# Kernel optimization log

Measured on AMD Instinct MI355X. Metric: run time of the kernel, lower is better.

The kernel has to match this reference:

```python
import jax, jax.numpy as jnp
import numpy as np
import math

B, N, H, NH, L, NC = 8, 128, 128, 4, 4, 1
DH = H // NH
EPS = 1e-5

def _gelu(x):
    return jax.nn.gelu(x, approximate=False)  # torch nn.GELU default is exact erf

def _ln(x, g, b):
    m = x.mean(-1, keepdims=True)
    v = ((x - m) ** 2).mean(-1, keepdims=True)
    return (x - m) / jnp.sqrt(v + EPS) * g + b

def _bn(x, mask, g, b):
    # BatchNorm1d over valid (unpadded) nodes only, batch statistics (train mode)
    m = mask[..., None].astype(x.dtype)
    cnt = m.sum()
    mu = (x * m).sum((0, 1)) / cnt
    var = (((x - mu) ** 2) * m).sum((0, 1)) / cnt
    return (x - mu) / jnp.sqrt(var + EPS) * g + b

def _forward(e, u, atom_emb, bond_emb, eigw_W, eigw_b, mha_norm_g, mha_norm_b, qkv_W, qkv_b, out_W, out_b, ffn_norm_g, ffn_norm_b, ffn1_W, ffn1_b, ffn2_W, ffn2_b, dec_W, dec_b, fe1_W, fe1_b, fe2_W, fe2_b, pre_W, pre_b, f1_W, f1_b, bn1_g, bn1_b, f2_W, f2_b, bn2_g, bn2_b, lin_W, lin_b, node_feat, edge_feat, length):
    Bx, Nx = e.shape
    node_mask = jnp.arange(Nx)[None, :] < length[:, None]                        # [B,N]
    edge_mask = (node_mask[:, :, None] & node_mask[:, None, :]).astype(e.dtype)  # [B,src,dst]
    # SineEncoding
    div = jnp.exp(jnp.arange(0, H, 2, dtype=e.dtype) * (-math.log(10000.0) / H))
    pe = (e * 100.0)[:, :, None] * div
    eeig = jnp.concatenate([e[..., None], jnp.sin(pe), jnp.cos(pe)], axis=-1)    # [B,N,H+1]
    eig = eeig @ eigw_W.T + eigw_b                                               # [B,N,H]
    # multi-head self-attention over eigenvalue tokens with key padding mask
    xm = _ln(eig, mha_norm_g, mha_norm_b)
    qkv = xm @ qkv_W.T + qkv_b
    q, k, v = jnp.split(qkv, 3, axis=-1)
    q = q.reshape(Bx, Nx, NH, DH).transpose(0, 2, 1, 3)
    k = k.reshape(Bx, Nx, NH, DH).transpose(0, 2, 1, 3)
    v = v.reshape(Bx, Nx, NH, DH).transpose(0, 2, 1, 3)
    scores = jnp.einsum('bhqd,bhkd->bhqk', q, k) / math.sqrt(DH)
    scores = jnp.where(node_mask[:, None, None, :], scores, -jnp.inf)
    attn = jax.nn.softmax(scores, axis=-1)                                       # [B,NH,N,N]
    ctx = jnp.einsum('bhqk,bhkd->bhqd', attn, v).transpose(0, 2, 1, 3).reshape(Bx, Nx, H)
    eig = eig + (ctx @ out_W.T + out_b)
    y = _ln(eig, ffn_norm_g, ffn_norm_b)
    y = _gelu(y @ ffn1_W.T + ffn1_b) @ ffn2_W.T + ffn2_b
    eig = eig + y
    new_e = (eig @ dec_W.T + dec_b).transpose(0, 2, 1)                           # [B,NH,N]
    # spectral bases: identity + u @ diag(new_e_k) @ u^T per head, as fused diagonal scale
    filters = jnp.einsum('bnm,bkm,bpm->bnpk', u, new_e, u)                       # [B,N,N,NH]
    eye = jnp.broadcast_to(jnp.eye(Nx, dtype=e.dtype)[None, :, :, None], (Bx, Nx, Nx, 1))
    bases = jnp.concatenate([eye, filters], axis=-1)                             # [B,N,N,NH+1]
    bases = _gelu(_gelu(bases @ fe1_W.T + fe1_b) @ fe2_W.T + fe2_b)              # [B,N,N,H]
    xf = atom_emb[node_feat]                                                     # [B,N,H]
    ea = bond_emb[edge_feat]                                                     # [B,N,N,H]
    for l in range(L):
        # copy_u gather + per-edge FFN * bases + masked scatter-sum to dst
        msg = _gelu((xf[:, :, None, :] + ea) @ pre_W[l].T + pre_b[l]) * bases
        aggr = jnp.einsum('bijh,bij->bjh', msg, edge_mask)
        xf = xf + aggr
        y = xf @ f1_W[l].T + f1_b[l]
        y = jax.nn.relu(_bn(y, node_mask, bn1_g[l], bn1_b[l]))
        y = y @ f2_W[l].T + f2_b[l]
        y = jax.nn.relu(_bn(y, node_mask, bn2_g[l], bn2_b[l]))
        xf = xf + y
    nm = node_mask[..., None].astype(e.dtype)
    h = (xf * nm).sum(1) / length[:, None].astype(e.dtype)                       # AvgPooling over valid nodes
    h = h @ lin_W.T + lin_b
    return h, new_e, attn

def setup_inputs():
    key = jax.random.key(0)
    ks = iter(jax.random.split(key, 64))
    def w(*shape):
        return jax.random.normal(next(ks), shape, dtype=jnp.float32) * 0.02
    z = lambda *s: jnp.zeros(s, dtype=jnp.float32)
    o = lambda *s: jnp.ones(s, dtype=jnp.float32)
    e = jax.random.uniform(next(ks), (B, N), dtype=jnp.float32) * 2.0
    u = jnp.linalg.qr(jax.random.normal(next(ks), (B, N, N), dtype=jnp.float32))[0]
    inp = {
        'e': e, 'u': u,
        'atom_emb': w(40, H), 'bond_emb': w(10, H).at[0].set(0.0),
        'eigw_W': w(H, H + 1), 'eigw_b': z(H),
        'mha_norm_g': o(H), 'mha_norm_b': z(H),
        'qkv_W': w(3 * H, H), 'qkv_b': z(3 * H),
        'out_W': w(H, H), 'out_b': z(H),
        'ffn_norm_g': o(H), 'ffn_norm_b': z(H),
        'ffn1_W': w(H, H), 'ffn1_b': z(H),
        'ffn2_W': w(H, H), 'ffn2_b': z(H),
        'dec_W': w(NH, H), 'dec_b': z(NH),
        'fe1_W': w(H, NH + 1), 'fe1_b': z(H),
        'fe2_W': w(H, H), 'fe2_b': z(H),
        'pre_W': w(L, H, H), 'pre_b': z(L, H),
        'f1_W': w(L, H, H), 'f1_b': z(L, H),
        'bn1_g': o(L, H), 'bn1_b': z(L, H),
        'f2_W': w(L, H, H), 'f2_b': z(L, H),
        'bn2_g': o(L, H), 'bn2_b': z(L, H),
        'lin_W': w(NC, H), 'lin_b': z(NC),
        'node_feat': jax.random.randint(next(ks), (B, N), 0, 40),
        'edge_feat': jax.random.randint(next(ks), (B, N, N), 0, 10),
        'length': 64 + jax.random.randint(next(ks), (B,), 0, N - 63),
    }
    return inp

def reference(e, u, atom_emb, bond_emb, eigw_W, eigw_b, mha_norm_g, mha_norm_b, qkv_W, qkv_b, out_W, out_b, ffn_norm_g, ffn_norm_b, ffn1_W, ffn1_b, ffn2_W, ffn2_b, dec_W, dec_b, fe1_W, fe1_b, fe2_W, fe2_b, pre_W, pre_b, f1_W, f1_b, bn1_g, bn1_b, f2_W, f2_b, bn2_g, bn2_b, lin_W, lin_b, node_feat, edge_feat, length):
    return _forward(e, u, atom_emb, bond_emb, eigw_W, eigw_b, mha_norm_g, mha_norm_b, qkv_W, qkv_b, out_W, out_b, ffn_norm_g, ffn_norm_b, ffn1_W, ffn1_b, ffn2_W, ffn2_b, dec_W, dec_b, fe1_W, fe1_b, fe2_W, fe2_b, pre_W, pre_b, f1_W, f1_b, bn1_g, bn1_b, f2_W, f2_b, bn2_g, bn2_b, lin_W, lin_b, node_feat, edge_feat, length)
```

## Files before the change

### kernel.cpp

```cpp
#include <hip/hip_runtime.h>
#include <hip/hip_bf16.h>
#include <math.h>

#define BB 8
#define NN 128
#define HH 128
#define NHD 4
#define DHD 32
#define LAY 4
#define EPSV 1e-5f

typedef __hip_bfloat16 bf16;
typedef unsigned short ushortt;
typedef short bf16x8 __attribute__((ext_vector_type(8)));
typedef float f32x4 __attribute__((ext_vector_type(4)));

__device__ __forceinline__ float b2f(bf16 x){ return __bfloat162float(x); }
__device__ __forceinline__ bf16 f2b(float x){ return __float2bfloat16(x); }
__device__ __forceinline__ ushortt f2us(float x){ bf16 b=__float2bfloat16(x); return *(ushortt*)&b; }
__device__ __forceinline__ float gelu_f(float x){ return 0.5f*x*(1.0f+erff(x*0.7071067811865476f)); }
__device__ __forceinline__ float gelu_h(float x){
  float t = 0.7978845608028654f*x*(1.0f + 0.044715f*x*x);
  float e = __expf(2.0f*t);
  float th = 1.0f - 2.0f/(e + 1.0f);
  return 0.5f*x*(1.0f + th);
}
__device__ __forceinline__ float erf_fast(float x){
  float ax = fabsf(x);
  float t = __builtin_amdgcn_rcpf(__builtin_fmaf(0.3275911f, ax, 1.0f));
  float p = __builtin_fmaf(1.061405429f, t, -1.453152027f);
  p = __builtin_fmaf(p, t, 1.421413741f);
  p = __builtin_fmaf(p, t, -0.284496736f);
  p = __builtin_fmaf(p, t, 0.254829592f);
  p = p*t;
  float e = __expf(-ax*ax);
  float y = __builtin_fmaf(-p, e, 1.0f);
  return __builtin_copysignf(y, x);
}
__device__ __forceinline__ float gelu_fe(float x){
  return 0.5f*x*(1.0f + erf_fast(x*0.7071067811865476f));
}


__global__ __launch_bounds__(256) void k_prep(const float* __restrict__ fe2W,
    const float* __restrict__ preW, const float* __restrict__ eigW,
    const float* __restrict__ qkvW, const float* __restrict__ outW,
    const float* __restrict__ ffn1W, const float* __restrict__ ffn2W,
    const float* __restrict__ f1W, const float* __restrict__ f2W,
    const float* __restrict__ aemb, const int* __restrict__ nf,
    const float* __restrict__ bemb, const float* __restrict__ preb,
    ushortt* __restrict__ wbf, float* __restrict__ gs, float* __restrict__ xf0,
    float* __restrict__ eigWT, float* __restrict__ qkvWT, float* __restrict__ outWT,
    float* __restrict__ ffn1WT, float* __restrict__ ffn2WT,
    float* __restrict__ f1WT, float* __restrict__ f2WT,
    float* __restrict__ bondWall){
  int idx = blockIdx.x*256 + threadIdx.x;
  if (idx < 10240) gs[idx] = 0.f;
  if (idx < 81920){
    float v = (idx < 16384) ? fe2W[idx] : preW[idx - 16384];
    wbf[idx] = f2us(v);
  }
  if (idx < 131072){
    int node = idx >> 7, h2 = idx & 127;
    xf0[idx] = aemb[nf[node]*HH + h2];
  }
  if (idx < 16512){ int o = idx/129, kq = idx - o*129; eigWT[kq*128+o] = eigW[idx]; }
  if (idx < 49152){ int o = idx>>7, m = idx&127; qkvWT[m*384+o] = qkvW[idx]; }
  if (idx < 16384){ int o = idx>>7, m = idx&127;
    outWT[m*128+o]  = outW[idx];
    ffn1WT[m*128+o] = ffn1W[idx];
    ffn2WT[m*128+o] = ffn2W[idx];
  }
  if (idx < 65536){ int l = idx>>14, r = idx&16383; int o = r>>7, m = r&127;
    f1WT[l*16384 + m*128+o] = f1W[idx];
    f2WT[l*16384 + m*128+o] = f2W[idx];
  }
  if (idx < 5120){
    int l = idx / 1280; int r = idx - l*1280; int e2 = r >> 7; int hcol = r & 127;
    const float* br = bemb + e2*128;
    const float* wr = preW + l*16384 + hcol*128;
    float acc = preb[l*128 + hcol];
    for (int m=0;m<128;m++) acc += br[m]*wr[m];
    bondWall[idx] = acc;
  }
}


__global__ void k_fe_a(const float* __restrict__ e, const float* __restrict__ eigWT,
                       const float* __restrict__ eigb, const float* __restrict__ g,
                       const float* __restrict__ bt, const float* __restrict__ qkvWT,
                       const float* __restrict__ qkvb,
                       float* __restrict__ eigout, float* __restrict__ q,
                       float* __restrict__ kT, float* __restrict__ v){
  int row = blockIdx.x; int tid = threadIdx.x;
  int b = row >> 7, n = row & 127;
  __shared__ float ee[129]; __shared__ float buf[128]; __shared__ float xm[128];
  float ev = e[row];
  if (tid < 64){
    float dv = expf(-0.1439115683121279f * (float)tid);
    float pe = ev * 100.0f * dv;
    ee[1+tid] = sinf(pe);
    ee[65+tid] = cosf(pe);
  }
  if (tid == 0) ee[0] = ev;
  __syncthreads();
  float x = eigb[tid];
  for (int k2=0;k2<129;k2++) x += ee[k2]*eigWT[k2*128+tid];
  eigout[row*HH+tid] = x;
  buf[tid]=x; __syncthreads();
  for (int s2=64;s2>0;s2>>=1){ if(tid<s2) buf[tid]+=buf[tid+s2]; __syncthreads(); }
  float mean = buf[0]*(1.0f/128.0f); __syncthreads();
  float d = x-mean; buf[tid]=d*d; __syncthreads();
  for (int s2=64;s2>0;s2>>=1){ if(tid<s2) buf[tid]+=buf[tid+s2]; __syncthreads(); }
  float var = buf[0]*(1.0f/128.0f);
  xm[tid] = d*rsqrtf(var+EPSV)*g[tid]+bt[tid];
  __syncthreads();
  #pragma unroll
  for (int s3=0;s3<3;s3++){
    float acc = qkvb[s3*HH+tid];
    const float* wt = qkvWT + s3*HH + tid;
    for (int m=0;m<HH;m++) acc += xm[m]*wt[m*384];
    if (s3==0) q[row*HH+tid]=acc;
    else if (s3==1) kT[b*16384 + tid*128 + n]=acc;
    else v[row*HH+tid]=acc;
  }
}

__global__ __launch_bounds__(512) void k_attc(const float* __restrict__ q,
    const float* __restrict__ kT, const float* __restrict__ v,
    const float* __restrict__ eig, const int* __restrict__ length,
    const float* __restrict__ outWT, const float* __restrict__ outb,
    const float* __restrict__ fng, const float* __restrict__ fnb,
    const float* __restrict__ w1T, const float* __restrict__ b1,
    const float* __restrict__ w2T, const float* __restrict__ b2,
    const float* __restrict__ dW, const float* __restrict__ db,
    float* __restrict__ newe, float* __restrict__ outp){
  int row = blockIdx.x; int b = row>>7, qi = row&127;
  int tid = threadIdx.x;
  int hg = tid>>7, lt = tid&127;
  int len = length[b];
  __shared__ float qv[4][DHD];
  __shared__ float red[4][128];
  __shared__ float satt[4][128];
  __shared__ float part[4][128];
  __shared__ float sc[128], sbuf[128], sxm[128], stt[128], sx[128];
  if (lt < DHD) qv[hg][lt] = q[(b*NN+qi)*HH + hg*DHD + lt];
  __syncthreads();
  float s = -1e30f;
  if (lt < len){
    const float* kr = kT + b*16384 + hg*DHD*128 + lt;
    float scr=0.f;
    for (int d2=0; d2<DHD; d2++) scr += qv[hg][d2]*kr[d2*128];
    s = scr * 0.17677669529663687f;
  }
  red[hg][lt]=s; __syncthreads();
  for (int st=64;st>0;st>>=1){ if(lt<st) red[hg][lt]=fmaxf(red[hg][lt],red[hg][lt+st]); __syncthreads(); }
  float mx = red[hg][0]; __syncthreads();
  float pp = (lt<len)? expf(s-mx):0.0f;
  red[hg][lt]=pp; __syncthreads();
  for (int st=64;st>0;st>>=1){ if(lt<st) red[hg][lt]+=red[hg][lt+st]; __syncthreads(); }
  float a = pp / red[hg][0];
  satt[hg][lt] = a;
  outp[4104 + ((b*NHD+hg)*NN+qi)*NN + lt] = a;
  __syncthreads();
  {
    int hd = lt>>5;
    float p=0.f;
    for (int j=hg*32; j<hg*32+32; j++) p += satt[hd][j]*v[(b*NN+j)*HH+lt];
    part[hg][lt]=p;
  }
  __syncthreads();
  if (tid < 128) sc[tid] = (part[0][tid]+part[1][tid])+(part[2][tid]+part[3][tid]);
  __syncthreads();
  {
    float p = (hg==0)? outb[lt] : 0.f;
    for (int m=hg*32; m<hg*32+32; m++) p += sc[m]*outWT[m*128+lt];
    part[hg][lt]=p;
  }
  __syncthreads();
  if (tid < 128){
    float x = eig[row*HH+tid] + ((part[0][tid]+part[1][tid])+(part[2][tid]+part[3][tid]));
    sx[tid] = x; sbuf[tid] = x;
  }
  __syncthreads();
  for (int s2=64;s2>0;s2>>=1){ if(tid<s2) sbuf[tid]+=sbuf[tid+s2]; __syncthreads(); }
  float mean = sbuf[0]*(1.f/128.f); __syncthreads();
  if (tid < 128){ float d = sx[tid]-mean; sbuf[tid]=d*d; }
  __syncthreads();
  for (int s2=64;s2>0;s2>>=1){ if(tid<s2) sbuf[tid]+=sbuf[tid+s2]; __syncthreads(); }
  float var = sbuf[0]*(1.f/128.f);
  if (tid < 128){
    float d = sx[tid]-mean;
    sxm[tid] = d*rsqrtf(var+EPSV)*fng[tid]+fnb[tid];
  }
  __syncthreads();
  {
    float p = (hg==0)? b1[lt] : 0.f;
    for (int m=hg*32; m<hg*32+32; m++) p += sxm[m]*w1T[m*128+lt];
    part[hg][lt]=p;
  }
  __syncthreads();
  if (tid < 128) stt[tid]=gelu_f((part[0][tid]+part[1][tid])+(part[2][tid]+part[3][tid]));
  __syncthreads();
  {
    float p = (hg==0)? b2[lt] : 0.f;
    for (int m=hg*32; m<hg*32+32; m++) p += stt[m]*w2T[m*128+lt];
    part[hg][lt]=p;
  }
  __syncthreads();
  if (tid < 128) sx[tid] = sx[tid] + ((part[0][tid]+part[1][tid])+(part[2][tid]+part[3][tid]));
  __syncthreads();
  if (tid < 4){
    float acc = db[tid];
    const float* wr = dW + tid*HH;
    for (int h2=0;h2<HH;h2++) acc += sx[h2]*wr[h2];
    int idx=(b*NHD+tid)*NN+qi;
    newe[idx]=acc; outp[8+idx]=acc;
  }
}

__global__ __launch_bounds__(256) void k_fe2(const float* __restrict__ u,
    const float* __restrict__ newe,
    const float* __restrict__ w1g, const float* __restrict__ b1g,
    const ushortt* __restrict__ w2bf, const float* __restrict__ b2g,
    const int* __restrict__ length,
    bf16* __restrict__ bases){
  int blk = blockIdx.x;
  int bi = blk >> 1;
  int r0 = (blk & 1)*64;
  int b = bi >> 7;
  int nloc = bi & 127;
  int len = length[b];
  if (nloc >= len || r0 >= len) return;
  int tid = threadIdx.x;
  int lane = tid & 63, w = tid >> 6, quad = lane >> 4, l15 = lane & 15;
  int pr = r0 + w*16 + l15;
  __shared__ alignas(16) ushortt sW2[128*128];
  __shared__ float w1a[128*4];
  __shared__ float w1b[128*2];
  __shared__ float b2s[128];
  __shared__ float cn[4][128];
  for (int idx = tid; idx < 2048; idx += 256){
    int r = idx >> 4, cb = idx & 15;
    *(uint4*)&sW2[r*128 + ((cb*8) ^ ((r&15)<<3))] = *(const uint4*)&w2bf[r*128 + cb*8];
  }
  if (tid < 128){
    w1a[tid*4+0] = b1g[tid];
    w1a[tid*4+1] = w1g[tid*5+0];
    w1a[tid*4+2] = w1g[tid*5+1];
    w1a[tid*4+3] = w1g[tid*5+2];
    w1b[tid*2+0] = w1g[tid*5+3];
    w1b[tid*2+1] = w1g[tid*5+4];
    b2s[tid] = b2g[tid];
  }
  for (int idx = tid; idx < 512; idx += 256){
    int k = idx >> 7, m = idx & 127;
    cn[k][m] = u[(b*NN+nloc)*NN + m] * newe[(b*NHD+k)*NN + m];
  }
  __syncthreads();
  bool wact = (r0 + w*16) < len;
  f32x4 acc[8];
  #pragma unroll
  for (int nt=0;nt<8;nt++) acc[nt] = (f32x4){0.f,0.f,0.f,0.f};
  if (wact){
    float f0=0.f, f1=0.f, f2v=0.f, f3=0.f;
    const float4* ur = (const float4*)(u + ((size_t)b*NN + pr)*NN);
    for (int m4 = quad*8; m4 < quad*8+8; m4++){
      float4 uv = ur[m4];
      int m = m4*4;
      f0 += cn[0][m]*uv.x; f0 += cn[0][m+1]*uv.y; f0 += cn[0][m+2]*uv.z; f0 += cn[0][m+3]*uv.w;
      f1 += cn[1][m]*uv.x; f1 += cn[1][m+1]*uv.y; f1 += cn[1][m+2]*uv.z; f1 += cn[1][m+3]*uv.w;
      f2v += cn[2][m]*uv.x; f2v += cn[2][m+1]*uv.y; f2v += cn[2][m+2]*uv.z; f2v += cn[2][m+3]*uv.w;
      f3 += cn[3][m]*uv.x; f3 += cn[3][m+1]*uv.y; f3 += cn[3][m+2]*uv.z; f3 += cn[3][m+3]*uv.w;
    }
    f0 += __shfl_xor(f0, 16, 64);  f0 += __shfl_xor(f0, 32, 64);
    f1 += __shfl_xor(f1, 16, 64);  f1 += __shfl_xor(f1, 32, 64);
    f2v += __shfl_xor(f2v, 16, 64); f2v += __shfl_xor(f2v, 32, 64);
    f3 += __shfl_xor(f3, 16, 64);  f3 += __shfl_xor(f3, 32, 64);
    float dg = (pr == nloc) ? 1.0f : 0.0f;
    for (int kk = 0; kk < 128; kk += 32){
      bf16x8 af;
      #pragma unroll
      for (int j=0;j<8;j++){
        int m = kk + quad*8 + j;
        const float4 wa = *(const float4*)&w1a[m*4];
        const float2 wb = *(const float2*)&w1b[m*2];
        float a = wa.x + wa.y*dg + wa.z*f0 + wa.w*f1 + wb.x*f2v + wb.y*f3;
        af[j] = (short)f2us(gelu_fe(a));
      }
      #pragma unroll
      for (int nt=0;nt<8;nt++){
        int rowb = nt*16 + l15;
        int off = (kk + quad*8) ^ (l15 << 3);
        bf16x8 bfr = *(const bf16x8*)&sW2[rowb*128 + off];
        acc[nt] = __builtin_amdgcn_mfma_f32_16x16x32_bf16(af, bfr, acc[nt], 0, 0, 0);
      }
    }
  }
  __syncthreads();
  ushortt* sT = sW2;
  if (wact){
    #pragma unroll
    for (int nt=0;nt<8;nt++){
      int h = nt*16 + l15;
      float bb = b2s[h];
      #pragma unroll
      for (int reg=0;reg<4;reg++){
        int lr = w*16 + quad*4 + reg;
        sT[lr*132 + h] = f2us(gelu_fe(acc[nt][reg] + bb));
      }
    }
  }
  __syncthreads();
  int rmax = len - r0; if (rmax > 64) rmax = 64;
  ushort4* gout = (ushort4*)(bases + (size_t)bi*16384 + r0*128);
  for (int idx = tid; idx < rmax*32; idx += 256){
    int row = idx >> 5, seg = idx & 31;
    gout[idx] = *(const ushort4*)&sT[row*132 + seg*4];
  }
}


__global__ __launch_bounds__(256) void k_xwl2(const float* __restrict__ xfprev,
    const float* __restrict__ t2, const float* __restrict__ gsum2p,
    const float* __restrict__ gsq2p, const float* __restrict__ g2p,
    const float* __restrict__ bb2p, const int* __restrict__ length, int prevapply,
    const ushortt* __restrict__ wbfl, float* __restrict__ xfB,
    float* __restrict__ xfW){
  int blk = blockIdx.x;
  int b = blk >> 2, rq = blk & 3;
  int tid = threadIdx.x;
  int lane = tid & 63, w = tid >> 6, quad = lane >> 4, l15 = lane & 15;
  __shared__ alignas(16) ushortt sA[32*136];
  __shared__ float smu[128], sistd[128], sg[128], sbb[128];
  if (prevapply && tid < 128){
    float cnt = 0.f;
    for (int q2=0;q2<BB;q2++) cnt += (float)length[q2];
    float mu = gsum2p[tid]/cnt;
    float var = gsq2p[tid]/cnt - mu*mu;
    smu[tid]=mu; sistd[tid]=rsqrtf(fmaxf(var,0.0f)+EPSV);
    sg[tid]=g2p[tid]; sbb[tid]=bb2p[tid];
  }
  __syncthreads();
  for (int idx = tid; idx < 1024; idx += 256){
    int r = idx >> 5, c = idx & 31;
    int gr = b*128 + rq*32 + r;
    float4 xv = ((const float4*)xfprev)[gr*32 + c];
    if (prevapply){
      float4 tv = ((const float4*)t2)[gr*32 + c];
      int f0 = c*4;
      xv.x += fmaxf((tv.x-smu[f0+0])*sistd[f0+0]*sg[f0+0]+sbb[f0+0], 0.f);
      xv.y += fmaxf((tv.y-smu[f0+1])*sistd[f0+1]*sg[f0+1]+sbb[f0+1], 0.f);
      xv.z += fmaxf((tv.z-smu[f0+2])*sistd[f0+2]*sg[f0+2]+sbb[f0+2], 0.f);
      xv.w += fmaxf((tv.w-smu[f0+3])*sistd[f0+3]*sg[f0+3]+sbb[f0+3], 0.f);
      ((float4*)xfB)[gr*32 + c] = xv;
    }
    ushort4 o;
    o.x=f2us(xv.x); o.y=f2us(xv.y); o.z=f2us(xv.z); o.w=f2us(xv.w);
    *(ushort4*)&sA[r*136 + c*4] = o;
  }
  __syncthreads();
  f32x4 acc[2][2];
  #pragma unroll
  for (int mt=0;mt<2;mt++)
    #pragma unroll
    for (int nt=0;nt<2;nt++) acc[mt][nt] = (f32x4){0.f,0.f,0.f,0.f};
  #pragma unroll
  for (int kk = 0; kk < 128; kk += 32){
    bf16x8 af[2], bfr[2];
    #pragma unroll
    for (int mt=0;mt<2;mt++) af[mt] = *(const bf16x8*)&sA[(mt*16+l15)*136 + kk + quad*8];
    #pragma unroll
    for (int nt=0;nt<2;nt++) bfr[nt] = *(const bf16x8*)&wbfl[((w*2+nt)*16+l15)*128 + kk + quad*8];
    #pragma unroll
    for (int mt=0;mt<2;mt++)
      #pragma unroll
      for (int nt=0;nt<2;nt++)
        acc[mt][nt] = __builtin_amdgcn_mfma_f32_16x16x32_bf16(af[mt], bfr[nt], acc[mt][nt], 0, 0, 0);
  }
  #pragma unroll
  for (int mt=0;mt<2;mt++)
    #pragma unroll
    for (int nt=0;nt<2;nt++){
      int h = (w*2+nt)*16 + l15;
      #pragma unroll
      for (int reg=0;reg<4;reg++){
        int prr = rq*32 + mt*16 + quad*4 + reg;
        xfW[(b*128 + prr)*128 + h] = acc[mt][nt][reg];
      }
    }
}

__global__ __launch_bounds__(512) void k_edge(const float* __restrict__ xfin, float* __restrict__ xfout,
    const bf16* __restrict__ bases, const float* __restrict__ xfW,
    const float* __restrict__ bondWl, const int* __restrict__ ef,
    const int* __restrict__ length,
    const float* __restrict__ w1t, const float* __restrict__ bias1,
    float* __restrict__ t1, float* __restrict__ gst){
  int bj = blockIdx.x; int b = bj >> 7, j = bj & 127;
  int len = length[b];
  int tid = threadIdx.x; int h = tid & 127, ih = tid >> 7;
  __shared__ float sBW[10][128];
  __shared__ int sEf[128];
  __shared__ float part[4][128];
  for (int idx = tid; idx < 1280; idx += 512) sBW[idx>>7][idx&127] = bondWl[idx];
  if (tid < 128) sEf[tid] = ef[(b*NN + tid)*NN + j];
  __syncthreads();
  float agg = 0.f;
  if (j < len){
    const float* xwb = xfW + b*NN*HH + h;
    const bf16* bb = bases + ((size_t)b*NN + j)*NN*HH + h;
    for (int i = ih; i < len; i += 4){
      float vv = gelu_h(xwb[i*128] + sBW[sEf[i]][h]);
      agg += vv * b2f(bb[i*128]);
    }
  }
  part[ih][h] = agg; __syncthreads();
  if (tid < 128){
    int o = (b*NN + j)*HH + tid;
    float xrow = xfin[o] + part[0][tid] + part[1][tid] + part[2][tid] + part[3][tid];
    xfout[o] = xrow;
    part[0][tid] = xrow;
  }
  __syncthreads();
  float acc = (ih==0) ? bias1[h] : 0.f;
  {
    const float* wcol = w1t + h;
    int m0 = ih*32;
    for (int m = m0; m < m0+32; m++) acc += part[0][m]*wcol[m*128];
  }
  float* red = &sBW[0][0];
  __syncthreads();
  red[ih*128 + h] = acc; __syncthreads();
  if (tid < 128){
    float t1v = red[tid] + red[128+tid] + red[256+tid] + red[384+tid];
    t1[(b*NN + j)*HH + tid] = t1v;
    if (j < len){
      int bank = bj & 7;
      atomicAdd(&gst[bank*256 + tid], t1v);
      atomicAdd(&gst[bank*256 + 128 + tid], t1v*t1v);
    }
  }
}

__global__ __launch_bounds__(256) void k_g2s(const float* __restrict__ t1,
    const float* __restrict__ gstL,
    const float* __restrict__ g1, const float* __restrict__ bb1,
    const float* __restrict__ w2t, const float* __restrict__ bias2,
    const int* __restrict__ length, float* __restrict__ t2){
  int blk = blockIdx.x; int tid = threadIdx.x;
  int f = tid & 127, rh = tid >> 7;
  __shared__ float sy[4][128];
  __shared__ float red1[2][128], red2[2][128];
  int r0 = blk*4;
  float cnt = 0.f;
  for (int b=0;b<BB;b++) cnt += (float)length[b];
  float su = 0.f, sq = 0.f;
  #pragma unroll
  for (int k=0;k<8;k++){ su += gstL[k*256 + f]; sq += gstL[k*256 + 128 + f]; }
  float mu = su/cnt;
  float var = sq/cnt - mu*mu;
  float istd = rsqrtf(fmaxf(var,0.0f)+EPSV);
  float gg = g1[f], bbv = bb1[f];
  for (int idx = tid; idx < 512; idx += 256){
    int r = idx >> 7;
    float x = t1[(r0+r)*128 + f];
    float y = (x-mu)*istd*gg + bbv;
    sy[r][f] = fmaxf(y, 0.0f);
  }
  __syncthreads();
  float bsv = bias2[f];
  float s=0.f, s2=0.f;
  for (int rr = rh*2; rr < rh*2+2; rr++){
    int rg = r0 + rr; int b = rg >> 7, n = rg & 127;
    float acc = bsv;
    for (int m=0;m<128;m++) acc += sy[rr][m]*w2t[m*128+f];
    t2[rg*128+f] = acc;
    if (n < length[b]){ s += acc; s2 += acc*acc; }
  }
  red1[rh][f]=s; red2[rh][f]=s2; __syncthreads();
  if (tid < 128){
    atomicAdd((float*)&gstL[2048 + tid], red1[0][tid]+red1[1][tid]);
    atomicAdd((float*)&gstL[2048 + 128 + tid], red2[0][tid]+red2[1][tid]);
  }
}

__global__ void k_pool2(const float* __restrict__ xf, const float* __restrict__ t2,
                        const float* __restrict__ gsum2, const float* __restrict__ gsq2,
                        const float* __restrict__ g2, const float* __restrict__ bb2,
                        const int* __restrict__ length,
                        const float* lw, const float* lb, float* __restrict__ outp){
  int b = blockIdx.x, tid=threadIdx.x;
  int len = length[b];
  float cnt = 0.f;
  for (int q2=0;q2<BB;q2++) cnt += (float)length[q2];
  float mu = gsum2[tid]/cnt;
  float var = gsq2[tid]/cnt - mu*mu;
  float istd = rsqrtf(fmaxf(var,0.0f)+EPSV);
  float gg = g2[tid], bbv = bb2[tid];
  float s=0.f;
  for (int n2=0;n2<len;n2++){
    int o = (b*NN+n2)*HH+tid;
    float x = xf[o] + fmaxf((t2[o]-mu)*istd*gg+bbv, 0.0f);
    s += x;
  }
  s /= (float)len;
  __shared__ float red[128];
  red[tid]=s*lw[tid]; __syncthreads();
  for (int st=64;st>0;st>>=1){ if(tid<st) red[tid]+=red[tid+st]; __syncthreads(); }
  if (tid==0) outp[b]=red[0]+lb[0];
}


extern "C" void kernel_launch(void* const* d_in, const int* in_sizes, int n_in,
                              void* d_out, int out_size, void* d_ws, size_t ws_size,
                              hipStream_t stream) {
  (void)in_sizes; (void)n_in; (void)out_size; (void)ws_size;
  const float* e        = (const float*)d_in[0];
  const float* u        = (const float*)d_in[1];
  const float* atom_emb = (const float*)d_in[2];
  const float* bond_emb = (const float*)d_in[3];
  const float* eigw_W   = (const float*)d_in[4];
  const float* eigw_b   = (const float*)d_in[5];
  const float* mng      = (const float*)d_in[6];
  const float* mnb      = (const float*)d_in[7];
  const float* qkvW     = (const float*)d_in[8];
  const float* qkvb     = (const float*)d_in[9];
  const float* outW     = (const float*)d_in[10];
  const float* outb     = (const float*)d_in[11];
  const float* fng      = (const float*)d_in[12];
  const float* fnb      = (const float*)d_in[13];
  const float* ffn1W    = (const float*)d_in[14];
  const float* ffn1b    = (const float*)d_in[15];
  const float* ffn2W    = (const float*)d_in[16];
  const float* ffn2b    = (const float*)d_in[17];
  const float* decW     = (const float*)d_in[18];
  const float* decb     = (const float*)d_in[19];
  const float* fe1W     = (const float*)d_in[20];
  const float* fe1b     = (const float*)d_in[21];
  const float* fe2W     = (const float*)d_in[22];
  const float* fe2b     = (const float*)d_in[23];
  const float* preW     = (const float*)d_in[24];
  const float* preb     = (const float*)d_in[25];
  const float* f1W      = (const float*)d_in[26];
  const float* f1b      = (const float*)d_in[27];
  const float* bn1g     = (const float*)d_in[28];
  const float* bn1b     = (const float*)d_in[29];
  const float* f2W      = (const float*)d_in[30];
  const float* f2b      = (const float*)d_in[31];
  const float* bn2g     = (const float*)d_in[32];
  const float* bn2b     = (const float*)d_in[33];
  const float* linW     = (const float*)d_in[34];
  const float* linb     = (const float*)d_in[35];
  const int* nodef      = (const int*)d_in[36];
  const int* edgef      = (const int*)d_in[37];
  const int* length     = (const int*)d_in[38];

  float* outp = (float*)d_out;

  char* p = (char*)d_ws;
  auto alloc = [&](size_t bytes)->void*{ void* r=(void*)p; p += (bytes+255)&~(size_t)255; return r; };
  const int TOK = BB*NN*HH;
  float* eig   = (float*)alloc(TOK*4);
  float* q     = (float*)alloc(TOK*4);
  float* kT    = (float*)alloc(TOK*4);
  float* v     = (float*)alloc(TOK*4);
  float* newe  = (float*)alloc(BB*NHD*NN*4);
  bf16*  bases = (bf16*) alloc((size_t)BB*NN*NN*HH*2);
  float* xf0   = (float*)alloc(TOK*4);
  float* xfB   = (float*)alloc(TOK*4);
  float* xfC   = (float*)alloc(TOK*4);
  float* xfD   = (float*)alloc(TOK*4);
  float* t1    = (float*)alloc(TOK*4);
  float* t2    = (float*)alloc(TOK*4);
  float* xfW   = (float*)alloc(TOK*4);
  float* gs    = (float*)alloc(10240*4);
  ushortt* wbf = (ushortt*)alloc(81920*2);
  float* eigWT = (float*)alloc(16512*4);
  float* qkvWT = (float*)alloc(49152*4);
  float* outWT = (float*)alloc(16384*4);
  float* ffn1WT= (float*)alloc(16384*4);
  float* ffn2WT= (float*)alloc(16384*4);
  float* f1WT  = (float*)alloc(65536*4);
  float* f2WT  = (float*)alloc(65536*4);
  float* bondWall = (float*)alloc(5120*4);

  k_prep<<<512, 256, 0, stream>>>(fe2W, preW, eigw_W, qkvW, outW, ffn1W, ffn2W,
                                  f1W, f2W, atom_emb, nodef, bond_emb, preb,
                                  wbf, gs, xf0, eigWT, qkvWT, outWT, ffn1WT,
                                  ffn2WT, f1WT, f2WT, bondWall);

  k_fe_a<<<BB*NN, 128, 0, stream>>>(e, eigWT, eigw_b, mng, mnb, qkvWT, qkvb, eig, q, kT, v);
  k_attc<<<BB*NN, 512, 0, stream>>>(q, kT, v, eig, length,
                                    outWT, outb, fng, fnb,
                                    ffn1WT, ffn1b, ffn2WT, ffn2b,
                                    decW, decb, newe, outp);

  k_fe2<<<2*BB*NN, 256, 0, stream>>>(u, newe, fe1W, fe1b, wbf, fe2b, length, bases);

  const float* xfprev = xf0;
  float* xfcur = xfC;
  for (int l=0;l<LAY;l++){
    const ushortt* wbfl = wbf + 16384 + l*16384;
    float* gsl = gs + l*2560;
    float* gsp = gs + (l-1)*2560;
    k_xwl2<<<BB*4, 256, 0, stream>>>(xfprev, t2,
                                   (l>0)? gsp+2048 : gs, (l>0)? gsp+2048+128 : gs,
                                   bn2g + (l>0? (l-1)*HH:0), bn2b + (l>0? (l-1)*HH:0),
                                   length, (l>0)?1:0,
                                   wbfl, xfB, xfW);
    const float* xin = (l==0)? xf0 : xfB;
    k_edge<<<BB*NN, 512, 0, stream>>>(xin, xfcur, bases, xfW, bondWall + l*1280,
                                      edgef, length,
                                      f1WT + l*16384, f1b + l*HH, t1, gsl);
    k_g2s<<<256, 256, 0, stream>>>(t1, gsl, bn1g + l*HH, bn1b + l*HH,
                                   f2WT + l*16384, f2b + l*HH, length, t2);
    xfprev = xfcur;
    xfcur = (xfcur == xfC) ? xfD : xfC;
  }
  k_pool2<<<BB, 128, 0, stream>>>(xfprev, t2, gs+3*2560+2048, gs+3*2560+2048+128,
                                  bn2g + 3*HH, bn2b + 3*HH, length, linW, linb, outp);
}
```

Before: 397.9 us.

## Merge prep with front encoder and fold layer-0 projection into basis kernel

The weight-prep kernel and the eigen-encoding/QKV kernel become one launch. Extra blocks handle two rows each and read the original untransposed eig and qkv weights, so the transposes of those two matrices are dropped. The layer-0 bf16 MFMA projection (xf0 × pre_W) is appended as extra blocks to the basis-construction kernel. That removes the layer-0 launch of k_xwl2 and its runtime prevapply branch. Fewer launches and less serialisation are traded for strided per-thread weight reads in the encoder part.

Measured after the change: 390.3 us. Within noise of the previous version (-1.9%).

```diff
diff --git a/kernel.cpp b/kernel.cpp
--- a/kernel.cpp
+++ b/kernel.cpp
@@ -42,87 +42,89 @@
 }
 
 
-__global__ __launch_bounds__(256) void k_prep(const float* __restrict__ fe2W,
-    const float* __restrict__ preW, const float* __restrict__ eigW,
-    const float* __restrict__ qkvW, const float* __restrict__ outW,
-    const float* __restrict__ ffn1W, const float* __restrict__ ffn2W,
-    const float* __restrict__ f1W, const float* __restrict__ f2W,
-    const float* __restrict__ aemb, const int* __restrict__ nf,
-    const float* __restrict__ bemb, const float* __restrict__ preb,
+__global__ __launch_bounds__(256) void k_front(
+    const float* __restrict__ fe2W, const float* __restrict__ preW,
+    const float* __restrict__ outW, const float* __restrict__ ffn1W,
+    const float* __restrict__ ffn2W, const float* __restrict__ f1W,
+    const float* __restrict__ f2W, const float* __restrict__ aemb,
+    const int* __restrict__ nf, const float* __restrict__ bemb,
+    const float* __restrict__ preb,
     ushortt* __restrict__ wbf, float* __restrict__ gs, float* __restrict__ xf0,
-    float* __restrict__ eigWT, float* __restrict__ qkvWT, float* __restrict__ outWT,
-    float* __restrict__ ffn1WT, float* __restrict__ ffn2WT,
-    float* __restrict__ f1WT, float* __restrict__ f2WT,
-    float* __restrict__ bondWall){
-  int idx = blockIdx.x*256 + threadIdx.x;
-  if (idx < 10240) gs[idx] = 0.f;
-  if (idx < 81920){
-    float v = (idx < 16384) ? fe2W[idx] : preW[idx - 16384];
-    wbf[idx] = f2us(v);
-  }
-  if (idx < 131072){
-    int node = idx >> 7, h2 = idx & 127;
-    xf0[idx] = aemb[nf[node]*HH + h2];
-  }
-  if (idx < 16512){ int o = idx/129, kq = idx - o*129; eigWT[kq*128+o] = eigW[idx]; }
-  if (idx < 49152){ int o = idx>>7, m = idx&127; qkvWT[m*384+o] = qkvW[idx]; }
-  if (idx < 16384){ int o = idx>>7, m = idx&127;
-    outWT[m*128+o]  = outW[idx];
-    ffn1WT[m*128+o] = ffn1W[idx];
-    ffn2WT[m*128+o] = ffn2W[idx];
-  }
-  if (idx < 65536){ int l = idx>>14, r = idx&16383; int o = r>>7, m = r&127;
-    f1WT[l*16384 + m*128+o] = f1W[idx];
-    f2WT[l*16384 + m*128+o] = f2W[idx];
-  }
-  if (idx < 5120){
-    int l = idx / 1280; int r = idx - l*1280; int e2 = r >> 7; int hcol = r & 127;
-    const float* br = bemb + e2*128;
-    const float* wr = preW + l*16384 + hcol*128;
-    float acc = preb[l*128 + hcol];
-    for (int m=0;m<128;m++) acc += br[m]*wr[m];
-    bondWall[idx] = acc;
-  }
-}
-
-
-__global__ void k_fe_a(const float* __restrict__ e, const float* __restrict__ eigWT,
-                       const float* __restrict__ eigb, const float* __restrict__ g,
-                       const float* __restrict__ bt, const float* __restrict__ qkvWT,
-                       const float* __restrict__ qkvb,
-                       float* __restrict__ eigout, float* __restrict__ q,
-                       float* __restrict__ kT, float* __restrict__ v){
-  int row = blockIdx.x; int tid = threadIdx.x;
+    float* __restrict__ outWT, float* __restrict__ ffn1WT, float* __restrict__ ffn2WT,
+    float* __restrict__ f1WT, float* __restrict__ f2WT, float* __restrict__ bondWall,
+    const float* __restrict__ e, const float* __restrict__ eigW,
+    const float* __restrict__ eigb, const float* __restrict__ g,
+    const float* __restrict__ bt, const float* __restrict__ qkvW,
+    const float* __restrict__ qkvb,
+    float* __restrict__ eigout, float* __restrict__ q,
+    float* __restrict__ kT, float* __restrict__ v){
+  int blk = blockIdx.x;
+  int tid = threadIdx.x;
+  if (blk < 512){
+    int idx = blk*256 + tid;
+    if (idx < 10240) gs[idx] = 0.f;
+    if (idx < 81920){
+      float vv = (idx < 16384) ? fe2W[idx] : preW[idx - 16384];
+      wbf[idx] = f2us(vv);
+    }
+    if (idx < 131072){
+      int node = idx >> 7, h2 = idx & 127;
+      xf0[idx] = aemb[nf[node]*HH + h2];
+    }
+    if (idx < 16384){ int o = idx>>7, m = idx&127;
+      outWT[m*128+o]  = outW[idx];
+      ffn1WT[m*128+o] = ffn1W[idx];
+      ffn2WT[m*128+o] = ffn2W[idx];
+    }
+    if (idx < 65536){ int l = idx>>14, r = idx&16383; int o = r>>7, m = r&127;
+      f1WT[l*16384 + m*128+o] = f1W[idx];
+      f2WT[l*16384 + m*128+o] = f2W[idx];
+    }
+    if (idx < 5120){
+      int l = idx / 1280; int r = idx - l*1280; int e2 = r >> 7; int hcol = r & 127;
+      const float* br = bemb + e2*128;
+      const float* wr = preW + l*16384 + hcol*128;
+      float acc = preb[l*128 + hcol];
+      for (int m=0;m<128;m++) acc += br[m]*wr[m];
+      bondWall[idx] = acc;
+    }
+    return;
+  }
+  int sub = tid >> 7, lt = tid & 127;
+  int row = (blk - 512)*2 + sub;
   int b = row >> 7, n = row & 127;
-  __shared__ float ee[129]; __shared__ float buf[128]; __shared__ float xm[128];
+  __shared__ float ee[2][129]; __shared__ float buf[2][128]; __shared__ float xm[2][128];
   float ev = e[row];
-  if (tid < 64){
-    float dv = expf(-0.1439115683121279f * (float)tid);
+  if (lt < 64){
+    float dv = expf(-0.1439115683121279f * (float)lt);
     float pe = ev * 100.0f * dv;
-    ee[1+tid] = sinf(pe);
-    ee[65+tid] = cosf(pe);
-  }
-  if (tid == 0) ee[0] = ev;
-  __syncthreads();
-  float x = eigb[tid];
-  for (int k2=0;k2<129;k2++) x += ee[k2]*eigWT[k2*128+tid];
-  eigout[row*HH+tid] = x;
-  buf[tid]=x; __syncthreads();
-  for (int s2=64;s2>0;s2>>=1){ if(tid<s2) buf[tid]+=buf[tid+s2]; __syncthreads(); }
-  float mean = buf[0]*(1.0f/128.0f); __syncthreads();
-  float d = x-mean; buf[tid]=d*d; __syncthreads();
-  for (int s2=64;s2>0;s2>>=1){ if(tid<s2) buf[tid]+=buf[tid+s2]; __syncthreads(); }
-  float var = buf[0]*(1.0f/128.0f);
-  xm[tid] = d*rsqrtf(var+EPSV)*g[tid]+bt[tid];
+    ee[sub][1+lt] = sinf(pe);
+    ee[sub][65+lt] = cosf(pe);
+  }
+  if (lt == 0) ee[sub][0] = ev;
+  __syncthreads();
+  float x = eigb[lt];
+  {
+    const float* er = eigW + lt*129;
+    for (int k2=0;k2<129;k2++) x += ee[sub][k2]*er[k2];
+  }
+  eigout[row*HH+lt] = x;
+  buf[sub][lt]=x; __syncthreads();
+  for (int s2=64;s2>0;s2>>=1){ if(lt<s2) buf[sub][lt]+=buf[sub][lt+s2]; __syncthreads(); }
+  float mean = buf[sub][0]*(1.0f/128.0f); __syncthreads();
+  float d = x-mean; buf[sub][lt]=d*d; __syncthreads();
+  for (int s2=64;s2>0;s2>>=1){ if(lt<s2) buf[sub][lt]+=buf[sub][lt+s2]; __syncthreads(); }
+  float var = buf[sub][0]*(1.0f/128.0f);
+  xm[sub][lt] = d*rsqrtf(var+EPSV)*g[lt]+bt[lt];
   __syncthreads();
   #pragma unroll
   for (int s3=0;s3<3;s3++){
-    float acc = qkvb[s3*HH+tid];
-    const float* wt = qkvWT + s3*HH + tid;
-    for (int m=0;m<HH;m++) acc += xm[m]*wt[m*384];
-    if (s3==0) q[row*HH+tid]=acc;
-    else if (s3==1) kT[b*16384 + tid*128 + n]=acc;
-    else v[row*HH+tid]=acc;
+    float acc = qkvb[s3*HH+lt];
+    const float* wt = qkvW + (s3*HH + lt)*128;
+    for (int m=0;m<HH;m++) acc += xm[sub][m]*wt[m];
+    if (s3==0) q[row*HH+lt]=acc;
+    else if (s3==1) kT[b*16384 + lt*128 + n]=acc;
+    else v[row*HH+lt]=acc;
   }
 }
 
@@ -219,27 +221,74 @@
   }
 }
 
-__global__ __launch_bounds__(256) void k_fe2(const float* __restrict__ u,
+__global__ __launch_bounds__(256) void k_bx(const float* __restrict__ u,
     const float* __restrict__ newe,
     const float* __restrict__ w1g, const float* __restrict__ b1g,
     const ushortt* __restrict__ w2bf, const float* __restrict__ b2g,
     const int* __restrict__ length,
-    bf16* __restrict__ bases){
+    bf16* __restrict__ bases,
+    const float* __restrict__ xf0, const ushortt* __restrict__ wbfl0,
+    float* __restrict__ xfW){
   int blk = blockIdx.x;
+  int tid = threadIdx.x;
+  int lane = tid & 63, w = tid >> 6, quad = lane >> 4, l15 = lane & 15;
+  __shared__ alignas(16) char us[38400];
+  if (blk >= 2048){
+    int blk2 = blk - 2048;
+    int b = blk2 >> 2, rq = blk2 & 3;
+    ushortt* sA = (ushortt*)us;
+    for (int idx = tid; idx < 1024; idx += 256){
+      int r = idx >> 5, c = idx & 31;
+      int gr = b*128 + rq*32 + r;
+      float4 xv = ((const float4*)xf0)[gr*32 + c];
+      ushort4 o;
+      o.x=f2us(xv.x); o.y=f2us(xv.y); o.z=f2us(xv.z); o.w=f2us(xv.w);
+      *(ushort4*)&sA[r*136 + c*4] = o;
+    }
+    __syncthreads();
+    f32x4 acc[2][2];
+    #pragma unroll
+    for (int mt=0;mt<2;mt++)
+      #pragma unroll
+      for (int nt=0;nt<2;nt++) acc[mt][nt] = (f32x4){0.f,0.f,0.f,0.f};
+    #pragma unroll
+    for (int kk = 0; kk < 128; kk += 32){
+      bf16x8 af[2], bfr[2];
+      #pragma unroll
+      for (int mt=0;mt<2;mt++) af[mt] = *(const bf16x8*)&sA[(mt*16+l15)*136 + kk + quad*8];
+      #pragma unroll
+      for (int nt=0;nt<2;nt++) bfr[nt] = *(const bf16x8*)&wbfl0[((w*2+nt)*16+l15)*128 + kk + quad*8];
+      #pragma unroll
+      for (int mt=0;mt<2;mt++)
+        #pragma unroll
+        for (int nt=0;nt<2;nt++)
+          acc[mt][nt] = __builtin_amdgcn_mfma_f32_16x16x32_bf16(af[mt], bfr[nt], acc[mt][nt], 0, 0, 0);
+    }
+    #pragma unroll
+    for (int mt=0;mt<2;mt++)
+      #pragma unroll
+      for (int nt=0;nt<2;nt++){
+        int h = (w*2+nt)*16 + l15;
+        #pragma unroll
+        for (int reg=0;reg<4;reg++){
+          int prr = rq*32 + mt*16 + quad*4 + reg;
+          xfW[(b*128 + prr)*128 + h] = acc[mt][nt][reg];
+        }
+      }
+    return;
+  }
   int bi = blk >> 1;
   int r0 = (blk & 1)*64;
   int b = bi >> 7;
   int nloc = bi & 127;
   int len = length[b];
   if (nloc >= len || r0 >= len) return;
-  int tid = threadIdx.x;
-  int lane = tid & 63, w = tid >> 6, quad = lane >> 4, l15 = lane & 15;
   int pr = r0 + w*16 + l15;
-  __shared__ alignas(16) ushortt sW2[128*128];
-  __shared__ float w1a[128*4];
-  __shared__ float w1b[128*2];
-  __shared__ float b2s[128];
-  __shared__ float cn[4][128];
+  ushortt* sW2 = (ushortt*)us;
+  float* w1a = (float*)(us + 32768);
+  float* w1b = (float*)(us + 34816);
+  float* b2s = (float*)(us + 35840);
+  float* cn  = (float*)(us + 36352);
   for (int idx = tid; idx < 2048; idx += 256){
     int r = idx >> 4, cb = idx & 15;
     *(uint4*)&sW2[r*128 + ((cb*8) ^ ((r&15)<<3))] = *(const uint4*)&w2bf[r*128 + cb*8];
@@ -255,7 +304,7 @@
   }
   for (int idx = tid; idx < 512; idx += 256){
     int k = idx >> 7, m = idx & 127;
-    cn[k][m] = u[(b*NN+nloc)*NN + m] * newe[(b*NHD+k)*NN + m];
+    cn[k*128+m] = u[(b*NN+nloc)*NN + m] * newe[(b*NHD+k)*NN + m];
   }
   __syncthreads();
   bool wact = (r0 + w*16) < len;
@@ -268,10 +317,10 @@
     for (int m4 = quad*8; m4 < quad*8+8; m4++){
       float4 uv = ur[m4];
       int m = m4*4;
-      f0 += cn[0][m]*uv.x; f0 += cn[0][m+1]*uv.y; f0 += cn[0][m+2]*uv.z; f0 += cn[0][m+3]*uv.w;
-      f1 += cn[1][m]*uv.x; f1 += cn[1][m+1]*uv.y; f1 += cn[1][m+2]*uv.z; f1 += cn[1][m+3]*uv.w;
-      f2v += cn[2][m]*uv.x; f2v += cn[2][m+1]*uv.y; f2v += cn[2][m+2]*uv.z; f2v += cn[2][m+3]*uv.w;
-      f3 += cn[3][m]*uv.x; f3 += cn[3][m+1]*uv.y; f3 += cn[3][m+2]*uv.z; f3 += cn[3][m+3]*uv.w;
+      f0 += cn[m]*uv.x; f0 += cn[m+1]*uv.y; f0 += cn[m+2]*uv.z; f0 += cn[m+3]*uv.w;
+      f1 += cn[128+m]*uv.x; f1 += cn[128+m+1]*uv.y; f1 += cn[128+m+2]*uv.z; f1 += cn[128+m+3]*uv.w;
+      f2v += cn[256+m]*uv.x; f2v += cn[256+m+1]*uv.y; f2v += cn[256+m+2]*uv.z; f2v += cn[256+m+3]*uv.w;
+      f3 += cn[384+m]*uv.x; f3 += cn[384+m+1]*uv.y; f3 += cn[384+m+2]*uv.z; f3 += cn[384+m+3]*uv.w;
     }
     f0 += __shfl_xor(f0, 16, 64);  f0 += __shfl_xor(f0, 32, 64);
     f1 += __shfl_xor(f1, 16, 64);  f1 += __shfl_xor(f1, 32, 64);
@@ -324,7 +373,7 @@
 __global__ __launch_bounds__(256) void k_xwl2(const float* __restrict__ xfprev,
     const float* __restrict__ t2, const float* __restrict__ gsum2p,
     const float* __restrict__ gsq2p, const float* __restrict__ g2p,
-    const float* __restrict__ bb2p, const int* __restrict__ length, int prevapply,
+    const float* __restrict__ bb2p, const int* __restrict__ length,
     const ushortt* __restrict__ wbfl, float* __restrict__ xfB,
     float* __restrict__ xfW){
   int blk = blockIdx.x;
@@ -333,7 +382,7 @@
   int lane = tid & 63, w = tid >> 6, quad = lane >> 4, l15 = lane & 15;
   __shared__ alignas(16) ushortt sA[32*136];
   __shared__ float smu[128], sistd[128], sg[128], sbb[128];
-  if (prevapply && tid < 128){
+  if (tid < 128){
     float cnt = 0.f;
     for (int q2=0;q2<BB;q2++) cnt += (float)length[q2];
     float mu = gsum2p[tid]/cnt;
@@ -346,15 +395,13 @@
     int r = idx >> 5, c = idx & 31;
     int gr = b*128 + rq*32 + r;
     float4 xv = ((const float4*)xfprev)[gr*32 + c];
-    if (prevapply){
-      float4 tv = ((const float4*)t2)[gr*32 + c];
-      int f0 = c*4;
-      xv.x += fmaxf((tv.x-smu[f0+0])*sistd[f0+0]*sg[f0+0]+sbb[f0+0], 0.f);
-      xv.y += fmaxf((tv.y-smu[f0+1])*sistd[f0+1]*sg[f0+1]+sbb[f0+1], 0.f);
-      xv.z += fmaxf((tv.z-smu[f0+2])*sistd[f0+2]*sg[f0+2]+sbb[f0+2], 0.f);
-      xv.w += fmaxf((tv.w-smu[f0+3])*sistd[f0+3]*sg[f0+3]+sbb[f0+3], 0.f);
-      ((float4*)xfB)[gr*32 + c] = xv;
-    }
+    float4 tv = ((const float4*)t2)[gr*32 + c];
+    int f0 = c*4;
+    xv.x += fmaxf((tv.x-smu[f0+0])*sistd[f0+0]*sg[f0+0]+sbb[f0+0], 0.f);
+    xv.y += fmaxf((tv.y-smu[f0+1])*sistd[f0+1]*sg[f0+1]+sbb[f0+1], 0.f);
+    xv.z += fmaxf((tv.z-smu[f0+2])*sistd[f0+2]*sg[f0+2]+sbb[f0+2], 0.f);
+    xv.w += fmaxf((tv.w-smu[f0+3])*sistd[f0+3]*sg[f0+3]+sbb[f0+3], 0.f);
+    ((float4*)xfB)[gr*32 + c] = xv;
     ushort4 o;
     o.x=f2us(xv.x); o.y=f2us(xv.y); o.z=f2us(xv.z); o.w=f2us(xv.w);
     *(ushort4*)&sA[r*136 + c*4] = o;
@@ -576,8 +623,6 @@
   float* xfW   = (float*)alloc(TOK*4);
   float* gs    = (float*)alloc(10240*4);
   ushortt* wbf = (ushortt*)alloc(81920*2);
-  float* eigWT = (float*)alloc(16512*4);
-  float* qkvWT = (float*)alloc(49152*4);
   float* outWT = (float*)alloc(16384*4);
   float* ffn1WT= (float*)alloc(16384*4);
   float* ffn2WT= (float*)alloc(16384*4);
@@ -585,18 +630,20 @@
   float* f2WT  = (float*)alloc(65536*4);
   float* bondWall = (float*)alloc(5120*4);
 
-  k_prep<<<512, 256, 0, stream>>>(fe2W, preW, eigw_W, qkvW, outW, ffn1W, ffn2W,
-                                  f1W, f2W, atom_emb, nodef, bond_emb, preb,
-                                  wbf, gs, xf0, eigWT, qkvWT, outWT, ffn1WT,
-                                  ffn2WT, f1WT, f2WT, bondWall);
-
-  k_fe_a<<<BB*NN, 128, 0, stream>>>(e, eigWT, eigw_b, mng, mnb, qkvWT, qkvb, eig, q, kT, v);
+  k_front<<<1024, 256, 0, stream>>>(fe2W, preW, outW, ffn1W, ffn2W,
+                                    f1W, f2W, atom_emb, nodef, bond_emb, preb,
+                                    wbf, gs, xf0, outWT, ffn1WT, ffn2WT,
+                                    f1WT, f2WT, bondWall,
+                                    e, eigw_W, eigw_b, mng, mnb, qkvW, qkvb,
+                                    eig, q, kT, v);
+
   k_attc<<<BB*NN, 512, 0, stream>>>(q, kT, v, eig, length,
                                     outWT, outb, fng, fnb,
                                     ffn1WT, ffn1b, ffn2WT, ffn2b,
                                     decW, decb, newe, outp);
 
-  k_fe2<<<2*BB*NN, 256, 0, stream>>>(u, newe, fe1W, fe1b, wbf, fe2b, length, bases);
+  k_bx<<<2048 + BB*4, 256, 0, stream>>>(u, newe, fe1W, fe1b, wbf, fe2b, length,
+                                        bases, xf0, wbf + 16384, xfW);
 
   const float* xfprev = xf0;
   float* xfcur = xfC;
@@ -604,11 +651,11 @@
     const ushortt* wbfl = wbf + 16384 + l*16384;
     float* gsl = gs + l*2560;
     float* gsp = gs + (l-1)*2560;
-    k_xwl2<<<BB*4, 256, 0, stream>>>(xfprev, t2,
-                                   (l>0)? gsp+2048 : gs, (l>0)? gsp+2048+128 : gs,
-                                   bn2g + (l>0? (l-1)*HH:0), bn2b + (l>0? (l-1)*HH:0),
-                                   length, (l>0)?1:0,
-                                   wbfl, xfB, xfW);
+    if (l > 0){
+      k_xwl2<<<BB*4, 256, 0, stream>>>(xfprev, t2, gsp+2048, gsp+2048+128,
+                                       bn2g + (l-1)*HH, bn2b + (l-1)*HH,
+                                       length, wbfl, xfB, xfW);
+    }
     const float* xin = (l==0)? xf0 : xfB;
     k_edge<<<BB*NN, 512, 0, stream>>>(xin, xfcur, bases, xfW, bondWall + l*1280,
                                       edgef, length,
```
